# Kernel tuning notes

Measured on AMD Instinct MI355X. Metric: run time of the kernel, lower is better.

The kernel has to match this reference:

```python
import jax, jax.numpy as jnp
import numpy as np

N = 10000      # nodes
E = 320000     # edges
F_IN = 33      # input node features
H = 32         # hidden
G = 64         # graphs in batch


def setup_inputs() -> dict:
    key = jax.random.key(0)
    ks = jax.random.split(key, 24)
    s = 0.1  # small init scale for numerical sanity
    inp = {
        "x": jax.random.normal(ks[0], (N, F_IN), jnp.float32),
        "edge_index": jax.random.randint(ks[1], (2, E), 0, N, jnp.int32),
        "edge_attr": jax.random.uniform(ks[2], (E, 1), jnp.float32),
        "batch": jnp.sort(jax.random.randint(ks[3], (N,), 0, G, jnp.int32)),
        # conv1: edge-MLP Linear(1 -> F_IN*H), root weight [F_IN,H], bias [H]
        "nn_w1": jax.random.normal(ks[4], (1, F_IN * H), jnp.float32) * s,
        "nn_b1": jax.random.normal(ks[5], (F_IN * H,), jnp.float32) * s,
        "root1": jax.random.normal(ks[6], (F_IN, H), jnp.float32) * s,
        "bias1": jnp.zeros((H,), jnp.float32),
        # conv2: edge-MLP Linear(1 -> H*H)
        "nn_w2": jax.random.normal(ks[7], (1, H * H), jnp.float32) * s,
        "nn_b2": jax.random.normal(ks[8], (H * H,), jnp.float32) * s,
        "root2": jax.random.normal(ks[9], (H, H), jnp.float32) * s,
        "bias2": jnp.zeros((H,), jnp.float32),
        # conv3
        "nn_w3": jax.random.normal(ks[10], (1, H * H), jnp.float32) * s,
        "nn_b3": jax.random.normal(ks[11], (H * H,), jnp.float32) * s,
        "root3": jax.random.normal(ks[12], (H, H), jnp.float32) * s,
        "bias3": jnp.zeros((H,), jnp.float32),
        # readout MLP: Linear(3H -> H), Linear(H -> 2)
        "lin1_w": jax.random.normal(ks[13], (3 * H, H), jnp.float32) * s,
        "lin1_b": jnp.zeros((H,), jnp.float32),
        "lin2_w": jax.random.normal(ks[14], (H, 2), jnp.float32) * s,
        "lin2_b": jnp.zeros((2,), jnp.float32),
    }
    return inp


def _nnconv(x, src, dst, edge_attr, nn_w, nn_b, root, bias):
    """PyG NNConv (aggr='add'): out_i = x_i @ root + bias + sum_{e: dst(e)=i} x_{src(e)} @ Theta(e_attr)."""
    in_dim, out_dim = root.shape
    # per-edge weight matrix from edge MLP: [E, in, out]
    W = (edge_attr @ nn_w + nn_b).reshape(-1, in_dim, out_dim)
    msg = jnp.einsum('ei,eio->eo', x[src], W)          # gather + per-edge small matmul
    agg = jax.ops.segment_sum(msg, dst, num_segments=N)  # scatter-add into targets
    return agg + x @ root + bias


def reference(x, edge_index, edge_attr, batch,
              nn_w1, nn_b1, root1, bias1,
              nn_w2, nn_b2, root2, bias2,
              nn_w3, nn_b3, root3, bias3,
              lin1_w, lin1_b, lin2_w, lin2_b):
    src, dst = edge_index[0], edge_index[1]
    h = jax.nn.relu(_nnconv(x, src, dst, edge_attr, nn_w1, nn_b1, root1, bias1))
    h = jax.nn.relu(_nnconv(h, src, dst, edge_attr, nn_w2, nn_b2, root2, bias2))
    h = jax.nn.relu(_nnconv(h, src, dst, edge_attr, nn_w3, nn_b3, root3, bias3))
    # global add / mean / max pooling over graphs
    add_p = jax.ops.segment_sum(h, batch, num_segments=G)
    cnt = jax.ops.segment_sum(jnp.ones((N, 1), h.dtype), batch, num_segments=G)
    mean_p = add_p / jnp.maximum(cnt, 1.0)
    max_p = jax.ops.segment_max(h, batch, num_segments=G)
    max_p = jnp.where(jnp.isfinite(max_p), max_p, 0.0)  # guard empty segments
    g = jnp.concatenate([add_p, mean_p, max_p], axis=1)  # [G, 3H]
    g = jax.nn.relu(g @ lin1_w + lin1_b)
    # dropout p=0.5 is identity in eval mode
    logits = g @ lin2_w + lin2_b
    return jax.nn.log_softmax(logits, axis=-1)
```

## Files before the change

kernel.cpp:

```cpp
#include <hip/hip_runtime.h>

constexpr int N_  = 10000;
constexpr int E_  = 320000;
constexpr int F1  = 33;
constexpr int H   = 32;
constexpr int G   = 64;
constexpr int CAP = 96;

constexpr int GRID = 1250;
constexpr int BT   = 256;

__device__ __forceinline__ unsigned bf16r(float x) {
    unsigned u = __float_as_uint(x);
    return (u + 0x7FFFu + ((u >> 16) & 1u)) >> 16;
}

struct Prm {
    const float* x; const int* ei; const float* ea; const int* batch;
    const float* A1; const float* B1; const float* R1; const float* z1;
    const float* A2; const float* B2; const float* R2; const float* z2;
    const float* A3; const float* B3; const float* R3; const float* z3;
    const float* l1w; const float* l1b; const float* l2w; const float* l2b;
    int* counts; int* startsP; unsigned* meta;
    unsigned* UVa; float* Ra; unsigned* UVb; float* Rb; float* Hs;
    float* out;
};

__global__ __launch_bounds__(BT, 5) void k_build(Prm p) {
    const int tid = threadIdx.x, bid = blockIdx.x;
    {
        int e = bid * BT + tid;
        int s = p.ei[e];
        int d = p.ei[E_ + e];
        float av = p.ea[e];
        int pos = atomicAdd(&p.counts[d], 1);
        p.meta[(size_t)d * CAP + pos] = (unsigned)s | (bf16r(av) << 16);
    }
    const int grp = tid >> 5, f = tid & 31;
    const int node = bid * 8 + grp;
    if (f == 0) {
        int b = p.batch[node];
        int bp = (node == 0) ? -1 : p.batch[node - 1];
        if (b != bp) p.startsP[b] = node + 1;
    }
    float u = 0.f, v = 0.f, r = p.z1[f];
    const float* xr = p.x + (size_t)node * F1;
    #pragma unroll
    for (int k = 0; k < F1; ++k) {
        float xv = xr[k];
        u = fmaf(xv, p.A1[k * H + f], u);
        v = fmaf(xv, p.B1[k * H + f], v);
        r = fmaf(xv, p.R1[k * H + f], r);
    }
    p.UVa[(node << 5) | f] = bf16r(u) | (bf16r(v) << 16);
    p.Ra [(node << 5) | f] = r;
}

template<int LAYER>
__global__ __launch_bounds__(BT, 5) void k_agg(Prm p) {
    __shared__ float wL[3][H * H];
    const int tid = threadIdx.x;

    const unsigned* UVin; const float* Rin; unsigned* UVout; float* Rout;
    if (LAYER == 1)      { UVin = p.UVa; Rin = p.Ra; UVout = p.UVb; Rout = p.Rb; }
    else if (LAYER == 2) { UVin = p.UVb; Rin = p.Rb; UVout = p.UVa; Rout = p.Ra; }
    else                 { UVin = p.UVa; Rin = p.Ra; UVout = nullptr; Rout = nullptr; }

    if (LAYER == 1) {
        for (int i = tid; i < H * H; i += BT) {
            wL[0][i] = p.A2[i]; wL[1][i] = p.B2[i]; wL[2][i] = p.R2[i];
        }
    } else if (LAYER == 2) {
        for (int i = tid; i < H * H; i += BT) {
            wL[0][i] = p.A3[i]; wL[1][i] = p.B3[i]; wL[2][i] = p.R3[i];
        }
    }
    if (LAYER < 3) __syncthreads();

    const int lane = tid & 63, wav = tid >> 6;
    const int l2 = lane & 31;
    const int rg = l2 >> 3;
    const int fq = l2 & 7;
    const int n = blockIdx.x * 8 + wav * 2 + (lane >> 5);
    const int dg = p.counts[n];
    const unsigned* mrow = p.meta + (size_t)n * CAP;
    unsigned m0 = mrow[l2], m1 = mrow[32 + l2], m2 = mrow[64 + l2];
    float r = Rin[(n << 5) | l2];

    float a0 = 0.f, a1 = 0.f, a2 = 0.f, a3 = 0.f;
    uint4 wq[6]; unsigned mq[6];

    auto issue = [&](unsigned mreg, int t, int sl) {
        int j = 4 * t + rg;
        unsigned mv = __shfl(mreg, (lane & 32) | (j & 31), 64);
        mq[sl] = mv;
        unsigned src = min(mv & 0xFFFFu, (unsigned)(N_ - 1));
        wq[sl] = *reinterpret_cast<const uint4*>(UVin + ((size_t)src << 5) + 4 * fq);
    };
    auto use = [&](int t, int sl) {
        unsigned mv = mq[sl]; uint4 w = wq[sl];
        float a = __uint_as_float(mv & 0xFFFF0000u);
        bool live = (4 * t + rg) < dg;
        float t0 = fmaf(a, __uint_as_float(w.x << 16), __uint_as_float(w.x & 0xFFFF0000u));
        float t1 = fmaf(a, __uint_as_float(w.y << 16), __uint_as_float(w.y & 0xFFFF0000u));
        float t2 = fmaf(a, __uint_as_float(w.z << 16), __uint_as_float(w.z & 0xFFFF0000u));
        float t3 = fmaf(a, __uint_as_float(w.w << 16), __uint_as_float(w.w & 0xFFFF0000u));
        if (live) { a0 += t0; a1 += t1; a2 += t2; a3 += t3; }
    };

    issue(m0, 0, 0); issue(m0, 1, 1); issue(m0, 2, 2);
    issue(m0, 3, 3); issue(m0, 4, 4); issue(m0, 5, 5);
    #pragma unroll
    for (int t = 0; t < 12; ++t) {
        use(t, t % 6);
        if (t + 6 < 12) issue((t + 6 <= 7) ? m0 : m1, t + 6, t % 6);
    }
    if (__any(dg > 48)) {
        #pragma unroll
        for (int t = 12; t < 16; ++t) issue(m1, t, t - 12);
        #pragma unroll
        for (int t = 12; t < 16; ++t) use(t, t - 12);
        if (__any(dg > 64)) {
            #pragma unroll
            for (int t = 16; t < 20; ++t) issue(m2, t, t - 16);
            #pragma unroll
            for (int t = 16; t < 20; ++t) use(t, t - 16);
            #pragma unroll
            for (int t = 20; t < 24; ++t) issue(m2, t, t - 20);
            #pragma unroll
            for (int t = 20; t < 24; ++t) use(t, t - 20);
        }
    }

    a0 += __shfl_xor(a0, 8);  a0 += __shfl_xor(a0, 16);
    a1 += __shfl_xor(a1, 8);  a1 += __shfl_xor(a1, 16);
    a2 += __shfl_xor(a2, 8);  a2 += __shfl_xor(a2, 16);
    a3 += __shfl_xor(a3, 8);  a3 += __shfl_xor(a3, 16);

    int rsrc = (lane & 32) | (l2 >> 2);
    float s0 = __shfl(a0, rsrc, 64), s1 = __shfl(a1, rsrc, 64);
    float s2 = __shfl(a2, rsrc, 64), s3 = __shfl(a3, rsrc, 64);
    int c = l2 & 3;
    float accf = (c == 0) ? s0 : (c == 1) ? s1 : (c == 2) ? s2 : s3;

    float h = fmaxf(r + accf, 0.f);

    if (LAYER == 3) {
        p.Hs[(n << 5) | l2] = h;
    } else {
        const float zf = (LAYER == 1) ? p.z2[l2] : p.z3[l2];
        float u = 0.f, v = 0.f, rn = zf;
        #pragma unroll
        for (int k = 0; k < H; ++k) {
            float hk = __shfl(h, k, 32);
            u  = fmaf(hk, wL[0][k * H + l2], u);
            v  = fmaf(hk, wL[1][k * H + l2], v);
            rn = fmaf(hk, wL[2][k * H + l2], rn);
        }
        UVout[(n << 5) | l2] = bf16r(u) | (bf16r(v) << 16);
        Rout [(n << 5) | l2] = rn;
    }
}

__global__ __launch_bounds__(BT, 5) void k_pool(Prm p) {
    __shared__ int   sst[G];
    __shared__ float gpl[3 * H];
    const int tid = threadIdx.x;
    const int g = blockIdx.x;
    if (tid < G) sst[tid] = p.startsP[tid];
    __syncthreads();
    int sp = sst[g];
    int s0 = 0, e0 = 0;
    if (sp != 0) {
        s0 = sp - 1;
        e0 = N_;
        for (int j = g + 1; j < G; ++j)
            if (sst[j]) { e0 = sst[j] - 1; break; }
    }
    int f = tid >> 3, oct = tid & 7;
    float sum = 0.f, mx = 0.f;
    for (int n = s0 + oct; n < e0; n += 8) {
        float w = p.Hs[(n << 5) | f];
        sum += w;
        mx = fmaxf(mx, w);
    }
    sum += __shfl_xor(sum, 1); mx = fmaxf(mx, __shfl_xor(mx, 1));
    sum += __shfl_xor(sum, 2); mx = fmaxf(mx, __shfl_xor(mx, 2));
    sum += __shfl_xor(sum, 4); mx = fmaxf(mx, __shfl_xor(mx, 4));
    if (oct == 0) {
        float c = fmaxf((float)(e0 - s0), 1.0f);
        gpl[f] = sum;
        gpl[H + f] = sum / c;
        gpl[2 * H + f] = mx;
    }
    __syncthreads();
    if (tid < 32) {
        float hacc = p.l1b[tid];
        #pragma unroll
        for (int k = 0; k < H; ++k) {
            hacc = fmaf(gpl[k],         p.l1w[k * H + tid], hacc);
            hacc = fmaf(gpl[H + k],     p.l1w[(H + k) * H + tid], hacc);
            hacc = fmaf(gpl[2 * H + k], p.l1w[(2 * H + k) * H + tid], hacc);
        }
        float hid = fmaxf(hacc, 0.f);
        float p0 = hid * p.l2w[tid * 2 + 0];
        float p1 = hid * p.l2w[tid * 2 + 1];
        #pragma unroll
        for (int o = 16; o; o >>= 1) {
            p0 += __shfl_xor(p0, o, 32);
            p1 += __shfl_xor(p1, o, 32);
        }
        if (tid == 0) {
            float l0 = p0 + p.l2b[0], l1 = p1 + p.l2b[1];
            float m = fmaxf(l0, l1);
            float lse = m + logf(expf(l0 - m) + expf(l1 - m));
            p.out[g * 2 + 0] = l0 - lse;
            p.out[g * 2 + 1] = l1 - lse;
        }
    }
}


extern "C" void kernel_launch(void* const* d_in, const int* in_sizes, int n_in,
                              void* d_out, int out_size, void* d_ws, size_t ws_size,
                              hipStream_t stream) {
    const float* x      = (const float*)d_in[0];
    const int*   ei     = (const int*)  d_in[1];
    const float* ea     = (const float*)d_in[2];
    const int*   batch  = (const int*)  d_in[3];
    const float* nn_w1  = (const float*)d_in[4];
    const float* nn_b1  = (const float*)d_in[5];
    const float* root1  = (const float*)d_in[6];
    const float* bias1  = (const float*)d_in[7];
    const float* nn_w2  = (const float*)d_in[8];
    const float* nn_b2  = (const float*)d_in[9];
    const float* root2  = (const float*)d_in[10];
    const float* bias2  = (const float*)d_in[11];
    const float* nn_w3  = (const float*)d_in[12];
    const float* nn_b3  = (const float*)d_in[13];
    const float* root3  = (const float*)d_in[14];
    const float* bias3  = (const float*)d_in[15];
    const float* lin1_w = (const float*)d_in[16];
    const float* lin1_b = (const float*)d_in[17];
    const float* lin2_w = (const float*)d_in[18];
    const float* lin2_b = (const float*)d_in[19];
    float* out = (float*)d_out;

    char* ws = (char*)d_ws;
    size_t off = 0;
    auto alloc = [&](size_t bytes) -> void* {
        void* p = ws + off;
        off += (bytes + 255) & ~(size_t)255;
        return p;
    };
    const size_t zbytes = N_ * sizeof(int) + G * sizeof(int);
    char* zchunk = (char*)alloc(zbytes);
    int* counts  = (int*)zchunk;
    int* startsP = (int*)(zchunk + N_ * sizeof(int));
    unsigned* meta = (unsigned*)alloc((size_t)N_ * CAP * sizeof(unsigned));
    unsigned* UVa = (unsigned*)alloc((size_t)N_ * H * sizeof(unsigned));
    float*    Ra  = (float*)   alloc((size_t)N_ * H * sizeof(float));
    unsigned* UVb = (unsigned*)alloc((size_t)N_ * H * sizeof(unsigned));
    float*    Rb  = (float*)   alloc((size_t)N_ * H * sizeof(float));
    float*    Hs  = (float*)   alloc((size_t)N_ * H * sizeof(float));

    Prm prm{ x, ei, ea, batch,
             nn_w1, nn_b1, root1, bias1,
             nn_w2, nn_b2, root2, bias2,
             nn_w3, nn_b3, root3, bias3,
             lin1_w, lin1_b, lin2_w, lin2_b,
             counts, startsP, meta, UVa, Ra, UVb, Rb, Hs, out };

    hipMemsetAsync(zchunk, 0, zbytes, stream);
    k_build <<<GRID, BT, 0, stream>>>(prm);
    k_agg<1><<<GRID, BT, 0, stream>>>(prm);
    k_agg<2><<<GRID, BT, 0, stream>>>(prm);
    k_agg<3><<<GRID, BT, 0, stream>>>(prm);
    k_pool  <<<G,    BT, 0, stream>>>(prm);
}
```

Baseline: 159.5 us.

## Fuse graph pooling into last aggregation layer via atomics, restage edge gather

```diff
diff --git a/kernel.cpp b/kernel.cpp
--- a/kernel.cpp
+++ b/kernel.cpp
@@ -22,7 +22,8 @@
     const float* A3; const float* B3; const float* R3; const float* z3;
     const float* l1w; const float* l1b; const float* l2w; const float* l2b;
     int* counts; int* startsP; unsigned* meta;
-    unsigned* UVa; float* Ra; unsigned* UVb; float* Rb; float* Hs;
+    unsigned* UVa; float* Ra; unsigned* UVb; float* Rb;
+    float* psum; unsigned* pmax;
     float* out;
 };
 
@@ -59,6 +60,7 @@
 template<int LAYER>
 __global__ __launch_bounds__(BT, 5) void k_agg(Prm p) {
     __shared__ float wL[3][H * H];
+    __shared__ float sh[8][H];
     const int tid = threadIdx.x;
 
     const unsigned* UVin; const float* Rin; unsigned* UVout; float* Rout;
@@ -70,12 +72,13 @@
         for (int i = tid; i < H * H; i += BT) {
             wL[0][i] = p.A2[i]; wL[1][i] = p.B2[i]; wL[2][i] = p.R2[i];
         }
+        __syncthreads();
     } else if (LAYER == 2) {
         for (int i = tid; i < H * H; i += BT) {
             wL[0][i] = p.A3[i]; wL[1][i] = p.B3[i]; wL[2][i] = p.R3[i];
         }
-    }
-    if (LAYER < 3) __syncthreads();
+        __syncthreads();
+    }
 
     const int lane = tid & 63, wav = tid >> 6;
     const int l2 = lane & 31;
@@ -84,11 +87,11 @@
     const int n = blockIdx.x * 8 + wav * 2 + (lane >> 5);
     const int dg = p.counts[n];
     const unsigned* mrow = p.meta + (size_t)n * CAP;
-    unsigned m0 = mrow[l2], m1 = mrow[32 + l2], m2 = mrow[64 + l2];
+    unsigned m0 = mrow[l2];
     float r = Rin[(n << 5) | l2];
 
     float a0 = 0.f, a1 = 0.f, a2 = 0.f, a3 = 0.f;
-    uint4 wq[6]; unsigned mq[6];
+    uint4 wq[8]; unsigned mq[8];
 
     auto issue = [&](unsigned mreg, int t, int sl) {
         int j = 4 * t + rg;
@@ -108,27 +111,30 @@
         if (live) { a0 += t0; a1 += t1; a2 += t2; a3 += t3; }
     };
 
-    issue(m0, 0, 0); issue(m0, 1, 1); issue(m0, 2, 2);
-    issue(m0, 3, 3); issue(m0, 4, 4); issue(m0, 5, 5);
     #pragma unroll
-    for (int t = 0; t < 12; ++t) {
-        use(t, t % 6);
-        if (t + 6 < 12) issue((t + 6 <= 7) ? m0 : m1, t + 6, t % 6);
-    }
-    if (__any(dg > 48)) {
-        #pragma unroll
-        for (int t = 12; t < 16; ++t) issue(m1, t, t - 12);
-        #pragma unroll
-        for (int t = 12; t < 16; ++t) use(t, t - 12);
-        if (__any(dg > 64)) {
+    for (int t = 0; t < 8; ++t) issue(m0, t, t);
+    const bool need1 = __any(dg > 32);
+    unsigned m1 = 0;
+    if (need1) m1 = mrow[32 + l2];
+    #pragma unroll
+    for (int t = 0; t < 8; ++t) use(t, t);
+    if (need1) {
+        #pragma unroll
+        for (int t = 8; t < 12; ++t) issue(m1, t, t - 8);
+        #pragma unroll
+        for (int t = 8; t < 12; ++t) use(t, t - 8);
+        if (__any(dg > 48)) {
             #pragma unroll
-            for (int t = 16; t < 20; ++t) issue(m2, t, t - 16);
+            for (int t = 12; t < 16; ++t) issue(m1, t, t - 12);
             #pragma unroll
-            for (int t = 16; t < 20; ++t) use(t, t - 16);
-            #pragma unroll
-            for (int t = 20; t < 24; ++t) issue(m2, t, t - 20);
-            #pragma unroll
-            for (int t = 20; t < 24; ++t) use(t, t - 20);
+            for (int t = 12; t < 16; ++t) use(t, t - 12);
+            if (__any(dg > 64)) {
+                unsigned m2 = mrow[64 + l2];
+                #pragma unroll
+                for (int t = 16; t < 24; ++t) issue(m2, t, t - 16);
+                #pragma unroll
+                for (int t = 16; t < 24; ++t) use(t, t - 16);
+            }
         }
     }
 
@@ -146,7 +152,27 @@
     float h = fmaxf(r + accf, 0.f);
 
     if (LAYER == 3) {
-        p.Hs[(n << 5) | l2] = h;
+        sh[wav * 2 + (lane >> 5)][l2] = h;
+        __syncthreads();
+        if (tid < 32) {
+            const int f = tid;
+            const int n0 = blockIdx.x * 8;
+            float s = 0.f, mx = 0.f;
+            int cg = p.batch[n0];
+            #pragma unroll
+            for (int i = 0; i < 8; ++i) {
+                int bg = p.batch[n0 + i];
+                if (bg != cg) {
+                    atomicAdd(&p.psum[cg * H + f], s);
+                    atomicMax(&p.pmax[cg * H + f], __float_as_uint(mx));
+                    s = 0.f; mx = 0.f; cg = bg;
+                }
+                float hv = sh[i][f];
+                s += hv; mx = fmaxf(mx, hv);
+            }
+            atomicAdd(&p.psum[cg * H + f], s);
+            atomicMax(&p.pmax[cg * H + f], __float_as_uint(mx));
+        }
     } else {
         const float zf = (LAYER == 1) ? p.z2[l2] : p.z3[l2];
         float u = 0.f, v = 0.f, rn = zf;
@@ -162,12 +188,12 @@
     }
 }
 
-__global__ __launch_bounds__(BT, 5) void k_pool(Prm p) {
+__global__ __launch_bounds__(64, 8) void k_read(Prm p) {
     __shared__ int   sst[G];
     __shared__ float gpl[3 * H];
     const int tid = threadIdx.x;
     const int g = blockIdx.x;
-    if (tid < G) sst[tid] = p.startsP[tid];
+    sst[tid] = p.startsP[tid];
     __syncthreads();
     int sp = sst[g];
     int s0 = 0, e0 = 0;
@@ -177,21 +203,13 @@
         for (int j = g + 1; j < G; ++j)
             if (sst[j]) { e0 = sst[j] - 1; break; }
     }
-    int f = tid >> 3, oct = tid & 7;
-    float sum = 0.f, mx = 0.f;
-    for (int n = s0 + oct; n < e0; n += 8) {
-        float w = p.Hs[(n << 5) | f];
-        sum += w;
-        mx = fmaxf(mx, w);
-    }
-    sum += __shfl_xor(sum, 1); mx = fmaxf(mx, __shfl_xor(mx, 1));
-    sum += __shfl_xor(sum, 2); mx = fmaxf(mx, __shfl_xor(mx, 2));
-    sum += __shfl_xor(sum, 4); mx = fmaxf(mx, __shfl_xor(mx, 4));
-    if (oct == 0) {
+    if (tid < 32) {
+        float sum = p.psum[g * H + tid];
+        float mx  = __uint_as_float(p.pmax[g * H + tid]);
         float c = fmaxf((float)(e0 - s0), 1.0f);
-        gpl[f] = sum;
-        gpl[H + f] = sum / c;
-        gpl[2 * H + f] = mx;
+        gpl[tid] = sum;
+        gpl[H + tid] = sum / c;
+        gpl[2 * H + tid] = mx;
     }
     __syncthreads();
     if (tid < 32) {
@@ -253,28 +271,31 @@
         off += (bytes + 255) & ~(size_t)255;
         return p;
     };
-    const size_t zbytes = N_ * sizeof(int) + G * sizeof(int);
+    const size_t zbytes = N_ * sizeof(int) + G * sizeof(int)
+                        + G * H * sizeof(float) + G * H * sizeof(unsigned);
     char* zchunk = (char*)alloc(zbytes);
-    int* counts  = (int*)zchunk;
-    int* startsP = (int*)(zchunk + N_ * sizeof(int));
+    int*      counts  = (int*)zchunk;
+    int*      startsP = (int*)(zchunk + N_ * sizeof(int));
+    float*    psum    = (float*)(zchunk + N_ * sizeof(int) + G * sizeof(int));
+    unsigned* pmax    = (unsigned*)(zchunk + N_ * sizeof(int) + G * sizeof(int)
+                                    + G * H * sizeof(float));
     unsigned* meta = (unsigned*)alloc((size_t)N_ * CAP * sizeof(unsigned));
     unsigned* UVa = (unsigned*)alloc((size_t)N_ * H * sizeof(unsigned));
     float*    Ra  = (float*)   alloc((size_t)N_ * H * sizeof(float));
     unsigned* UVb = (unsigned*)alloc((size_t)N_ * H * sizeof(unsigned));
     float*    Rb  = (float*)   alloc((size_t)N_ * H * sizeof(float));
-    float*    Hs  = (float*)   alloc((size_t)N_ * H * sizeof(float));
 
     Prm prm{ x, ei, ea, batch,
              nn_w1, nn_b1, root1, bias1,
              nn_w2, nn_b2, root2, bias2,
              nn_w3, nn_b3, root3, bias3,
              lin1_w, lin1_b, lin2_w, lin2_b,
-             counts, startsP, meta, UVa, Ra, UVb, Rb, Hs, out };
+             counts, startsP, meta, UVa, Ra, UVb, Rb, psum, pmax, out };
 
     hipMemsetAsync(zchunk, 0, zbytes, stream);
     k_build <<<GRID, BT, 0, stream>>>(prm);
     k_agg<1><<<GRID, BT, 0, stream>>>(prm);
     k_agg<2><<<GRID, BT, 0, stream>>>(prm);
     k_agg<3><<<GRID, BT, 0, stream>>>(prm);
-    k_pool  <<<G,    BT, 0, stream>>>(prm);
-}
+    k_read  <<<G,    64, 0, stream>>>(prm);
+}
```

Result: faster. 155.2 us (-2.7%).
